# Kernel tuning notes

Measured on AMD Instinct MI355X. Metric: run time of the kernel, lower is better.

Reference implementation:

```python
import jax, jax.numpy as jnp
import numpy as np

B, D_IN = 4096, 4096
TOTAL_NODES, OUT_NODES = 17384, 1000
HID = TOTAL_NODES - OUT_NODES  # 16384


def setup_inputs() -> dict:
    key = jax.random.key(0)
    k1, k2, k3, k4, k5 = jax.random.split(key, 5)
    s1 = 1.0 / np.sqrt(D_IN)
    s2 = 1.0 / np.sqrt(D_IN + HID)
    return {
        "x": jax.random.normal(k1, (B, D_IN), dtype=jnp.float32),
        "W1": jax.random.normal(k2, (HID, D_IN), dtype=jnp.float32) * s1,
        "b1": jax.random.normal(k3, (HID,), dtype=jnp.float32) * s1,
        "W2": jax.random.normal(k4, (OUT_NODES, D_IN + HID), dtype=jnp.float32) * s2,
        "b2": jax.random.normal(k5, (OUT_NODES,), dtype=jnp.float32) * s2,
    }


def reference(x, W1, b1, W2, b2):
    # layer1 + ReLU: [B, HID]
    h1 = jax.nn.relu(jnp.einsum("bd,hd->bh", x, W1) + b1)
    # concat input with hidden activations: [B, D_IN + HID]
    concat = jnp.concatenate([x, h1], axis=1)
    # layer2: [B, OUT_NODES]
    out = jnp.einsum("bc,oc->bo", concat, W2) + b2
    return out
```

## Files before the change

### kernel.cpp

```cpp
#include <hip/hip_runtime.h>
#include <cstdint>
#include <cstddef>


using u16 = unsigned short;

typedef __bf16 bf16x8 __attribute__((ext_vector_type(8)));
typedef float  f32x4  __attribute__((ext_vector_type(4)));

#define BM 128
#define BN 128
#define BK 32

#define GLOBAL_AS __attribute__((address_space(1)))
#define LDS_AS    __attribute__((address_space(3)))

__device__ __forceinline__ void async_load16(const void* gp, void* lp) {
    __builtin_amdgcn_global_load_lds((GLOBAL_AS void*)gp, (LDS_AS void*)lp, 16, 0, 0);
}

__device__ __forceinline__ u16 f2bf(float f) {
    union { float f; uint32_t u; } c; c.f = f;
    uint32_t u = c.u;
    u += 0x7FFFu + ((u >> 16) & 1u);
    return (u16)(u >> 16);
}

__device__ __forceinline__ int swz(int q, int row) { return q ^ ((row >> 1) & 3); }


__global__ void cvt_x_kernel(const float* __restrict__ x, u16* __restrict__ dst) {
    int idx = blockIdx.x * 256 + threadIdx.x;
    int row = idx >> 10;
    int c4  = (idx & 1023) << 2;
    float4 v = *(const float4*)&x[(size_t)row * 4096 + c4];
    ushort4 o;
    o.x = f2bf(v.x); o.y = f2bf(v.y); o.z = f2bf(v.z); o.w = f2bf(v.w);
    *(ushort4*)&dst[(size_t)row * 20480 + c4] = o;
}

__global__ void cvt_flat_kernel(const float* __restrict__ src, u16* __restrict__ dst) {
    int idx = blockIdx.x * 256 + threadIdx.x;
    float4 v = *(const float4*)&src[(size_t)idx * 4];
    ushort4 o;
    o.x = f2bf(v.x); o.y = f2bf(v.y); o.z = f2bf(v.z); o.w = f2bf(v.w);
    *(ushort4*)&dst[(size_t)idx * 4] = o;
}

__global__ void cvt_w2_kernel(const float* __restrict__ src, u16* __restrict__ dst) {
    int idx = blockIdx.x * 256 + threadIdx.x;
    int row = idx / 5120;
    int c4  = (idx % 5120) * 4;
    ushort4 o;
    if (row < 1000) {
        float4 v = *(const float4*)&src[(size_t)row * 20480 + c4];
        o.x = f2bf(v.x); o.y = f2bf(v.y); o.z = f2bf(v.z); o.w = f2bf(v.w);
    } else {
        o.x = 0; o.y = 0; o.z = 0; o.w = 0;
    }
    *(ushort4*)&dst[(size_t)row * 20480 + c4] = o;
}

template <int EPI, int SWZ>
__global__ __launch_bounds__(256, 2)
void gemm_bt_kernel(const u16* __restrict__ A, int lda,
                    const u16* __restrict__ B, int ldb,
                    int K,
                    const float* __restrict__ bias,
                    void* __restrict__ Cout, int ldc, size_t c_slab) {
    __shared__ __align__(16) u16 As[BM * BK];
    __shared__ __align__(16) u16 Bs[BN * BK];

    const int tid = threadIdx.x;

    int bx = blockIdx.x, by = blockIdx.y;
    if (SWZ) {
        const int lin    = by * (int)gridDim.x + bx;
        const int panel  = lin >> 7;
        const int within = lin & 127;
        bx = panel * 4 + (within >> 5);
        by = within & 31;
    }
    const int m0 = by * BM;
    const int n0 = bx * BN;
    const int kz = blockIdx.z;

    A += (size_t)kz * K;
    B += (size_t)kz * K;

    const int r0 = tid >> 2;
    const int q0 = swz(tid & 3, r0);
    const int r1 = r0 + 64;
    const int q1 = swz(tid & 3, r1);

    const u16* ag0 = A + (size_t)(m0 + r0) * lda + q0 * 8;
    const u16* ag1 = A + (size_t)(m0 + r1) * lda + q1 * 8;
    const u16* bg0 = B + (size_t)(n0 + r0) * ldb + q0 * 8;
    const u16* bg1 = B + (size_t)(n0 + r1) * ldb + q1 * 8;
    u16* al0 = &As[tid * 8];
    u16* al1 = &As[tid * 8 + 2048];
    u16* bl0 = &Bs[tid * 8];
    u16* bl1 = &Bs[tid * 8 + 2048];

    const int wave = tid >> 6;
    const int lane = tid & 63;
    const int wr   = (wave >> 1) * 64;
    const int wc   = (wave & 1) * 64;
    const int ln16 = lane & 15;
    const int quad = lane >> 4;

    int aoff[4], boff[4];
#pragma unroll
    for (int i = 0; i < 4; ++i) {
        const int ra = wr + i * 16 + ln16;
        aoff[i] = ra * BK + swz(quad, ra) * 8;
        const int rb = wc + i * 16 + ln16;
        boff[i] = rb * BK + swz(quad, rb) * 8;
    }

    f32x4 acc[4][4] = {};

    for (int k0 = 0; k0 < K; k0 += BK) {
        async_load16(ag0, al0);
        async_load16(ag1, al1);
        async_load16(bg0, bl0);
        async_load16(bg1, bl1);
        ag0 += BK; ag1 += BK; bg0 += BK; bg1 += BK;
        __syncthreads();

        bf16x8 a[4], b[4];
#pragma unroll
        for (int i = 0; i < 4; ++i) a[i] = *(const bf16x8*)&As[aoff[i]];
#pragma unroll
        for (int j = 0; j < 4; ++j) b[j] = *(const bf16x8*)&Bs[boff[j]];

#pragma unroll
        for (int i = 0; i < 4; ++i)
#pragma unroll
            for (int j = 0; j < 4; ++j)
                acc[i][j] = __builtin_amdgcn_mfma_f32_16x16x32_bf16(
                    a[i], b[j], acc[i][j], 0, 0, 0);

        __syncthreads();
    }

    if (EPI == 0) {
        u16* C = (u16*)Cout;
#pragma unroll
        for (int i = 0; i < 4; ++i) {
#pragma unroll
            for (int j = 0; j < 4; ++j) {
                const int col = n0 + wc + j * 16 + ln16;
                const float bv = bias[col];
#pragma unroll
                for (int r = 0; r < 4; ++r) {
                    const int row = m0 + wr + i * 16 + quad * 4 + r;
                    float v = acc[i][j][r] + bv;
                    v = v > 0.0f ? v : 0.0f;
                    C[(size_t)row * ldc + col] = f2bf(v);
                }
            }
        }
    } else {
        float* C = (float*)Cout + (size_t)kz * c_slab;
#pragma unroll
        for (int i = 0; i < 4; ++i) {
#pragma unroll
            for (int j = 0; j < 4; ++j) {
                const int col = n0 + wc + j * 16 + ln16;
#pragma unroll
                for (int r = 0; r < 4; ++r) {
                    const int row = m0 + wr + i * 16 + quad * 4 + r;
                    C[(size_t)row * ldc + col] = acc[i][j][r];
                }
            }
        }
    }
}

__global__ void reduce_out_kernel(const float* __restrict__ part,
                                  const float* __restrict__ b2,
                                  float* __restrict__ out) {
    const int idx = blockIdx.x * 256 + threadIdx.x;
    const int m  = idx / 250;
    const int n4 = (idx % 250) * 4;
    const size_t slab = (size_t)4096 * 1024;
    const size_t off = (size_t)m * 1024 + n4;
    float4 s  = *(const float4*)&part[off];
    float4 p1 = *(const float4*)&part[slab + off];
    float4 p2 = *(const float4*)&part[2 * slab + off];
    float4 p3 = *(const float4*)&part[3 * slab + off];
    float4 bv = *(const float4*)&b2[n4];
    s.x += p1.x + p2.x + p3.x + bv.x;
    s.y += p1.y + p2.y + p3.y + bv.y;
    s.z += p1.z + p2.z + p3.z + bv.z;
    s.w += p1.w + p2.w + p3.w + bv.w;
    *(float4*)&out[(size_t)m * 1000 + n4] = s;
}


extern "C" void kernel_launch(void* const* d_in, const int* in_sizes, int n_in,
                              void* d_out, int out_size, void* d_ws, size_t ws_size,
                              hipStream_t stream) {
    const float* x  = (const float*)d_in[0];
    const float* W1 = (const float*)d_in[1];
    const float* b1 = (const float*)d_in[2];
    const float* W2 = (const float*)d_in[3];
    const float* b2 = (const float*)d_in[4];
    float* out = (float*)d_out;

    u16* concat = (u16*)d_ws;
    u16* W1b = concat + (size_t)4096 * 20480;
    u16* W2b = W1b + (size_t)16384 * 4096;
    float* partials = (float*)W1b;

    cvt_x_kernel   <<<16384, 256, 0, stream>>>(x, concat);
    cvt_flat_kernel<<<65536, 256, 0, stream>>>(W1, W1b);
    cvt_w2_kernel  <<<20480, 256, 0, stream>>>(W2, W2b);

    dim3 g1(16384 / BN, 4096 / BM, 1);
    gemm_bt_kernel<0, 1><<<g1, 256, 0, stream>>>(
        concat, 20480, W1b, 4096, 4096, b1, concat + 4096, 20480, 0);

    dim3 g2(1024 / BN, 4096 / BM, 4);
    gemm_bt_kernel<1, 0><<<g2, 256, 0, stream>>>(
        concat, 20480, W2b, 20480, 5120, nullptr, partials, 1024,
        (size_t)4096 * 1024);

    reduce_out_kernel<<<4000, 256, 0, stream>>>(partials, b2, out);
}
```

Before: 1.368 ms.

## Use 256x256 tiles with 4-stage async LDS pipeline and XCD-aware swizzle

Replaces the 128x128 single-buffered GEMM with a 512-thread 256x256 tile kernel. Global-to-LDS async loads run three tiles ahead through a 4-slot ring, with manual vmcnt waits and raw barriers in place of __syncthreads. MFMA sections are wrapped in raised wave priority, and the grid swizzle is changed so that consecutive blocks on each XCD share panels for L2 reuse. The larger tiles raise arithmetic intensity, but they use 128KB of LDS and more accumulator registers per thread, which may limit occupancy to one block per CU despite the launch bound asking for two.

```diff
diff --git a/kernel.cpp b/kernel.cpp
--- a/kernel.cpp
+++ b/kernel.cpp
@@ -7,10 +7,6 @@
 
 typedef __bf16 bf16x8 __attribute__((ext_vector_type(8)));
 typedef float  f32x4  __attribute__((ext_vector_type(4)));
-
-#define BM 128
-#define BN 128
-#define BK 32
 
 #define GLOBAL_AS __attribute__((address_space(1)))
 #define LDS_AS    __attribute__((address_space(3)))
@@ -62,99 +58,115 @@
 }
 
 template <int EPI, int SWZ>
-__global__ __launch_bounds__(256, 2)
-void gemm_bt_kernel(const u16* __restrict__ A, int lda,
+__global__ __launch_bounds__(512, 2)
+void gemm256_kernel(const u16* __restrict__ A, int lda,
                     const u16* __restrict__ B, int ldb,
                     int K,
                     const float* __restrict__ bias,
                     void* __restrict__ Cout, int ldc, size_t c_slab) {
-    __shared__ __align__(16) u16 As[BM * BK];
-    __shared__ __align__(16) u16 Bs[BN * BK];
+    __shared__ __align__(16) u16 As[4 * 8192];
+    __shared__ __align__(16) u16 Bs[4 * 8192];
 
     const int tid = threadIdx.x;
 
     int bx = blockIdx.x, by = blockIdx.y;
     if (SWZ) {
-        const int lin    = by * (int)gridDim.x + bx;
-        const int panel  = lin >> 7;
-        const int within = lin & 127;
-        bx = panel * 4 + (within >> 5);
-        by = within & 31;
-    }
-    const int m0 = by * BM;
-    const int n0 = bx * BN;
+        const int lin   = by * (int)gridDim.x + bx;
+        const int xcd   = lin & 7;
+        const int wg    = xcd * 128 + (lin >> 3);
+        const int panel = wg >> 6;
+        const int within = wg & 63;
+        bx = (panel >> 1) * 8 + (within & 7);
+        by = (panel & 1) * 8 + (within >> 3);
+    }
+    const int m0 = by * 256;
+    const int n0 = bx * 256;
     const int kz = blockIdx.z;
 
     A += (size_t)kz * K;
     B += (size_t)kz * K;
 
-    const int r0 = tid >> 2;
-    const int q0 = swz(tid & 3, r0);
-    const int r1 = r0 + 64;
-    const int q1 = swz(tid & 3, r1);
-
-    const u16* ag0 = A + (size_t)(m0 + r0) * lda + q0 * 8;
-    const u16* ag1 = A + (size_t)(m0 + r1) * lda + q1 * 8;
-    const u16* bg0 = B + (size_t)(n0 + r0) * ldb + q0 * 8;
-    const u16* bg1 = B + (size_t)(n0 + r1) * ldb + q1 * 8;
-    u16* al0 = &As[tid * 8];
-    u16* al1 = &As[tid * 8 + 2048];
-    u16* bl0 = &Bs[tid * 8];
-    u16* bl1 = &Bs[tid * 8 + 2048];
+    const int sr = tid >> 2;
+    const int sq = tid & 3;
+    const int qg = swz(sq, sr);
+    const u16* ga0 = A + (size_t)(m0 + sr) * lda + qg * 8;
+    const u16* ga1 = ga0 + (size_t)128 * lda;
+    const u16* gb0 = B + (size_t)(n0 + sr) * ldb + qg * 8;
+    const u16* gb1 = gb0 + (size_t)128 * ldb;
+
+#define STAGE4(cb) do {                                  \
+        async_load16(ga0, &As[(cb) + tid * 8]);          \
+        async_load16(ga1, &As[(cb) + 4096 + tid * 8]);   \
+        async_load16(gb0, &Bs[(cb) + tid * 8]);          \
+        async_load16(gb1, &Bs[(cb) + 4096 + tid * 8]);   \
+        ga0 += 32; ga1 += 32; gb0 += 32; gb1 += 32;      \
+    } while (0)
 
     const int wave = tid >> 6;
+    const int wm   = wave >> 2;
+    const int wn   = wave & 3;
     const int lane = tid & 63;
-    const int wr   = (wave >> 1) * 64;
-    const int wc   = (wave & 1) * 64;
     const int ln16 = lane & 15;
     const int quad = lane >> 4;
 
-    int aoff[4], boff[4];
-#pragma unroll
-    for (int i = 0; i < 4; ++i) {
-        const int ra = wr + i * 16 + ln16;
-        aoff[i] = ra * BK + swz(quad, ra) * 8;
-        const int rb = wc + i * 16 + ln16;
-        boff[i] = rb * BK + swz(quad, rb) * 8;
-    }
-
-    f32x4 acc[4][4] = {};
-
-    for (int k0 = 0; k0 < K; k0 += BK) {
-        async_load16(ag0, al0);
-        async_load16(ag1, al1);
-        async_load16(bg0, bl0);
-        async_load16(bg1, bl1);
-        ag0 += BK; ag1 += BK; bg0 += BK; bg1 += BK;
-        __syncthreads();
-
-        bf16x8 a[4], b[4];
-#pragma unroll
-        for (int i = 0; i < 4; ++i) a[i] = *(const bf16x8*)&As[aoff[i]];
-#pragma unroll
-        for (int j = 0; j < 4; ++j) b[j] = *(const bf16x8*)&Bs[boff[j]];
-
-#pragma unroll
-        for (int i = 0; i < 4; ++i)
+    int aoff[8], boff[4];
+#pragma unroll
+    for (int i = 0; i < 8; ++i) {
+        const int ra = wm * 128 + i * 16 + ln16;
+        aoff[i] = ra * 32 + swz(quad, ra) * 8;
+    }
+#pragma unroll
+    for (int j = 0; j < 4; ++j) {
+        const int rb = wn * 64 + j * 16 + ln16;
+        boff[j] = rb * 32 + swz(quad, rb) * 8;
+    }
+
+    f32x4 acc[8][4] = {};
+
+    STAGE4(0);
+    STAGE4(8192);
+    STAGE4(16384);
+
+    const int NT = K >> 5;
+    for (int t = 0; t < NT; ++t) {
+        if (t < NT - 2)       asm volatile("s_waitcnt vmcnt(8)" ::: "memory");
+        else if (t == NT - 2) asm volatile("s_waitcnt vmcnt(4)" ::: "memory");
+        else                  asm volatile("s_waitcnt vmcnt(0)" ::: "memory");
+        asm volatile("s_barrier" ::: "memory");
+
+        const int cb = (t & 3) * 8192;
+        bf16x8 a[8], b[4];
+#pragma unroll
+        for (int i = 0; i < 8; ++i) a[i] = *(const bf16x8*)&As[cb + aoff[i]];
+#pragma unroll
+        for (int j = 0; j < 4; ++j) b[j] = *(const bf16x8*)&Bs[cb + boff[j]];
+
+        if (t + 3 < NT) STAGE4(((t + 3) & 3) * 8192);
+
+        __builtin_amdgcn_s_setprio(1);
+#pragma unroll
+        for (int i = 0; i < 8; ++i)
 #pragma unroll
             for (int j = 0; j < 4; ++j)
                 acc[i][j] = __builtin_amdgcn_mfma_f32_16x16x32_bf16(
                     a[i], b[j], acc[i][j], 0, 0, 0);
-
-        __syncthreads();
-    }
+        __builtin_amdgcn_s_setprio(0);
+
+        asm volatile("s_barrier" ::: "memory");
+    }
+#undef STAGE4
 
     if (EPI == 0) {
         u16* C = (u16*)Cout;
 #pragma unroll
-        for (int i = 0; i < 4; ++i) {
-#pragma unroll
-            for (int j = 0; j < 4; ++j) {
-                const int col = n0 + wc + j * 16 + ln16;
-                const float bv = bias[col];
+        for (int j = 0; j < 4; ++j) {
+            const int col = n0 + wn * 64 + j * 16 + ln16;
+            const float bv = bias[col];
+#pragma unroll
+            for (int i = 0; i < 8; ++i) {
 #pragma unroll
                 for (int r = 0; r < 4; ++r) {
-                    const int row = m0 + wr + i * 16 + quad * 4 + r;
+                    const int row = m0 + wm * 128 + i * 16 + quad * 4 + r;
                     float v = acc[i][j][r] + bv;
                     v = v > 0.0f ? v : 0.0f;
                     C[(size_t)row * ldc + col] = f2bf(v);
@@ -164,13 +176,13 @@
     } else {
         float* C = (float*)Cout + (size_t)kz * c_slab;
 #pragma unroll
-        for (int i = 0; i < 4; ++i) {
-#pragma unroll
-            for (int j = 0; j < 4; ++j) {
-                const int col = n0 + wc + j * 16 + ln16;
+        for (int j = 0; j < 4; ++j) {
+            const int col = n0 + wn * 64 + j * 16 + ln16;
+#pragma unroll
+            for (int i = 0; i < 8; ++i) {
 #pragma unroll
                 for (int r = 0; r < 4; ++r) {
-                    const int row = m0 + wr + i * 16 + quad * 4 + r;
+                    const int row = m0 + wm * 128 + i * 16 + quad * 4 + r;
                     C[(size_t)row * ldc + col] = acc[i][j][r];
                 }
             }
@@ -218,12 +230,12 @@
     cvt_flat_kernel<<<65536, 256, 0, stream>>>(W1, W1b);
     cvt_w2_kernel  <<<20480, 256, 0, stream>>>(W2, W2b);
 
-    dim3 g1(16384 / BN, 4096 / BM, 1);
-    gemm_bt_kernel<0, 1><<<g1, 256, 0, stream>>>(
+    dim3 g1(16384 / 256, 4096 / 256, 1);
+    gemm256_kernel<0, 1><<<g1, 512, 0, stream>>>(
         concat, 20480, W1b, 4096, 4096, b1, concat + 4096, 20480, 0);
 
-    dim3 g2(1024 / BN, 4096 / BM, 4);
-    gemm_bt_kernel<1, 0><<<g2, 256, 0, stream>>>(
+    dim3 g2(1024 / 256, 4096 / 256, 4);
+    gemm256_kernel<1, 0><<<g2, 512, 0, stream>>>(
         concat, 20480, W2b, 20480, 5120, nullptr, partials, 1024,
         (size_t)4096 * 1024);
 
```

Result: faster. 1.169 ms (-14.6%).
